# Kernel tuning notes

Hardware: AMD Instinct MI355X
Metric: run time of the kernel (lower is better)

The kernel has to match this reference:

```python
import jax, jax.numpy as jnp
import numpy as np

INITIAL_RADIUS = 1.0  # init_kwargs: initial_radius > 0 -> distance-softmax branch


def reference(xyz, sparse_xyz, sparse_flow, resol_factor, K):
    # xyz: [B,3,N], sparse_xyz: [B,3,M], sparse_flow: [B,3,M]
    q = jnp.transpose(xyz, (0, 2, 1))            # [B,N,3]
    p = jnp.transpose(sparse_xyz, (0, 2, 1))     # [B,M,3]
    flow = jnp.transpose(sparse_flow, (0, 2, 1))  # [B,M,3]

    sigma = INITIAL_RADIUS * resol_factor
    qs = q / sigma
    ps = p / sigma

    # pairwise Euclidean distances [B,N,M]
    sq = (jnp.sum(qs * qs, -1)[:, :, None]
          + jnp.sum(ps * ps, -1)[:, None, :]
          - 2.0 * jnp.einsum('bnc,bmc->bnm', qs, ps))
    dist = jnp.sqrt(jnp.maximum(sq, 1e-12))

    # K nearest: smallest distances
    neg_d, idx = jax.lax.top_k(-dist, K)          # [B,N,K]
    K_dist = -neg_d                               # [B,N,K]

    # gather flow of the K neighbors: [B,N,K,3]
    grouped_flow = jnp.take_along_axis(flow[:, None, :, :], idx[..., None], axis=2)

    # softmax over -distance along K, weighted sum
    K_w = jax.nn.softmax(-K_dist, axis=2)         # [B,N,K]
    dense_flow = jnp.sum(K_w[..., None] * grouped_flow, axis=2)  # [B,N,3]

    return jnp.transpose(dense_flow, (0, 2, 1))   # [B,3,N]


def setup_inputs() -> dict:
    key = jax.random.key(0)
    k1, k2, k3 = jax.random.split(key, 3)
    B, N, M = 4, 16384, 4096
    return {
        'xyz': jax.random.normal(k1, (B, 3, N), dtype=jnp.float32),
        'sparse_xyz': jax.random.normal(k2, (B, 3, M), dtype=jnp.float32),
        'sparse_flow': jax.random.normal(k3, (B, 3, M), dtype=jnp.float32),
        'resol_factor': 1,
        'K': 5,
    }
```

## Files before the change

kernel.cpp:

```cpp
#include <hip/hip_runtime.h>
#include <math.h>
#include <stdint.h>


#define KNN 5
#define GRID 8
#define NCELL (GRID * GRID * GRID)
#define SPAN_TH 64
#define SLICES 8
#define BLOCK (SLICES * 64)
#define EPSM 1e-3f

typedef unsigned int u32;

__device__ __forceinline__ float get_inv_sigma(const int* __restrict__ rf) {
    const int ri = rf[0];
    const float sigma = (ri >= 1 && ri <= 1000000) ? (float)ri : __int_as_float(ri);
    return 1.0f / sigma;
}

__device__ __forceinline__ float rfl_f(float v) {
    return __int_as_float(__builtin_amdgcn_readfirstlane(__float_as_int(v)));
}

__device__ __forceinline__ int cid1(float x, float lo, float ich) {
    const int c = (int)floorf((x - lo) * ich);
    return c < 0 ? 0 : (c > GRID - 1 ? GRID - 1 : c);
}

__device__ __forceinline__ int sp3(int v) {
    return (v & 1) | ((v & 2) << 2) | ((v & 4) << 4);
}

#define CE_FULL(k, ki, c, ci)                          \
    {                                                  \
        const bool sw = (c) < (k);                     \
        const float vmn = fminf(k, c);                 \
        const float vmx = fmaxf(k, c);                 \
        const u32 nki = sw ? (ci) : (ki);              \
        const u32 nci = sw ? (ki) : (ci);              \
        (k) = vmn; (c) = vmx; (ki) = nki; (ci) = nci;  \
    }
#define CE_LAST(k, ki, c, ci)                          \
    {                                                  \
        const bool sw = (c) < (k);                     \
        (ki) = sw ? (ci) : (ki);                       \
        (k) = fminf(k, c);                             \
    }

#define LAD(P, CI)                                     \
    {                                                  \
        float t_ = qx * (P).x;                         \
        t_ = fmaf(qy, (P).y, t_);                      \
        t_ = fmaf(qz, (P).z, t_);                      \
        float c_ = fmaf(-2.0f, t_, (P).w);             \
        u32 ci_ = (u32)(CI);                           \
        CE_FULL(e0, i0, c_, ci_)                       \
        CE_FULL(e1, i1, c_, ci_)                       \
        CE_FULL(e2, i2, c_, ci_)                       \
        CE_FULL(e3, i3, c_, ci_)                       \
        CE_LAST(e4, i4, c_, ci_)                       \
    }


__global__ __launch_bounds__(256)
void prep_kernel(const float* __restrict__ sxyz, const int* __restrict__ rf,
                 float4* __restrict__ pts, int M, int total) {
    const int t = blockIdx.x * 256 + threadIdx.x;
    if (t >= total) return;
    const float inv = get_inv_sigma(rf);
    const int b = t / M, m = t - b * M;
    const float* sb = sxyz + (size_t)b * 3 * M;
    const float x = sb[m] * inv;
    const float y = sb[M + m] * inv;
    const float z = sb[2 * M + m] * inv;
    pts[t] = make_float4(x, y, z, fmaf(x, x, fmaf(y, y, z * z)));
}

template <bool USE_PTS>
__global__ __launch_bounds__(BLOCK, 8)
void knn_kernel(const float* __restrict__ xyz,
                const float* __restrict__ sxyz,
                const float* __restrict__ sflow,
                const int* __restrict__ rf,
                const float4* __restrict__ pts,
                float* __restrict__ out,
                int N, int M) {
    __shared__ float sval_d[SLICES * KNN * 64];
    __shared__ u32   sval_i[SLICES * KNN * 64];

    const int tid  = threadIdx.x;
    const int lane = tid & 63;
    const int wid  = tid >> 6;
    const int swid = __builtin_amdgcn_readfirstlane(wid);
    const int gpb  = N / 64;
    const int b    = blockIdx.x / gpb;
    const int grp  = blockIdx.x - b * gpb;
    const int n    = grp * 64 + lane;

    const float inv = get_inv_sigma(rf);
    const float* qb = xyz + (size_t)b * 3 * N;
    const float qx = qb[n] * inv;
    const float qy = qb[N + n] * inv;
    const float qz = qb[2 * N + n] * inv;
    const float qq = fmaf(qx, qx, fmaf(qy, qy, qz * qz));

    const int CH = M / SLICES;
    const int j0 = swid * CH;

    float e0 = 1e30f, e1 = 1e30f, e2 = 1e30f, e3 = 1e30f, e4 = 1e30f;
    u32   i0 = 0, i1 = 0, i2 = 0, i3 = 0, i4 = 0;

    if constexpr (USE_PTS) {
        const float4* __restrict__ P = pts + (size_t)b * M + j0;
#pragma unroll 4
        for (int j = 0; j < CH; ++j) {
            const float4 p = P[j];
            LAD(p, j0 + j)
        }
    } else {
        const float* __restrict__ sb = sxyz + (size_t)b * 3 * M;
#pragma unroll 4
        for (int j = 0; j < CH; ++j) {
            const float px = sb[j0 + j] * inv;
            const float py = sb[M + j0 + j] * inv;
            const float pz = sb[2 * M + j0 + j] * inv;
            const float pw = fmaf(px, px, fmaf(py, py, pz * pz));
            const float4 p = make_float4(px, py, pz, pw);
            LAD(p, j0 + j)
        }
    }

    sval_d[(wid * KNN + 0) * 64 + lane] = e0;  sval_i[(wid * KNN + 0) * 64 + lane] = i0;
    sval_d[(wid * KNN + 1) * 64 + lane] = e1;  sval_i[(wid * KNN + 1) * 64 + lane] = i1;
    sval_d[(wid * KNN + 2) * 64 + lane] = e2;  sval_i[(wid * KNN + 2) * 64 + lane] = i2;
    sval_d[(wid * KNN + 3) * 64 + lane] = e3;  sval_i[(wid * KNN + 3) * 64 + lane] = i3;
    sval_d[(wid * KNN + 4) * 64 + lane] = e4;  sval_i[(wid * KNN + 4) * 64 + lane] = i4;
    __syncthreads();

    if (wid == 0) {
        float m0 = 1e30f, m1 = 1e30f, m2 = 1e30f, m3 = 1e30f, m4 = 1e30f;
        u32   g0 = 0, g1 = 0, g2 = 0, g3 = 0, g4 = 0;
#pragma unroll
        for (int w = 0; w < SLICES; ++w) {
#pragma unroll
            for (int k = 0; k < KNN; ++k) {
                float c = sval_d[(w * KNN + k) * 64 + lane];
                u32  ci = sval_i[(w * KNN + k) * 64 + lane];
                CE_FULL(m0, g0, c, ci)
                CE_FULL(m1, g1, c, ci)
                CE_FULL(m2, g2, c, ci)
                CE_FULL(m3, g3, c, ci)
                CE_LAST(m4, g4, c, ci)
            }
        }

        const float d0 = sqrtf(fmaxf(m0 + qq, 1e-12f));
        const float d1 = sqrtf(fmaxf(m1 + qq, 1e-12f));
        const float d2 = sqrtf(fmaxf(m2 + qq, 1e-12f));
        const float d3 = sqrtf(fmaxf(m3 + qq, 1e-12f));
        const float d4 = sqrtf(fmaxf(m4 + qq, 1e-12f));
        const float w0 = 1.0f;
        const float w1 = expf(d0 - d1);
        const float w2 = expf(d0 - d2);
        const float w3 = expf(d0 - d3);
        const float w4 = expf(d0 - d4);
        const float inv_wsum = 1.0f / (w0 + w1 + w2 + w3 + w4);

        const float* fb = sflow + (size_t)b * 3 * M;
        float ax = 0.f, ay = 0.f, az = 0.f;
        ax = fmaf(w0, fb[g0], ax); ay = fmaf(w0, fb[M + g0], ay); az = fmaf(w0, fb[2 * M + g0], az);
        ax = fmaf(w1, fb[g1], ax); ay = fmaf(w1, fb[M + g1], ay); az = fmaf(w1, fb[2 * M + g1], az);
        ax = fmaf(w2, fb[g2], ax); ay = fmaf(w2, fb[M + g2], ay); az = fmaf(w2, fb[2 * M + g2], az);
        ax = fmaf(w3, fb[g3], ax); ay = fmaf(w3, fb[M + g3], ay); az = fmaf(w3, fb[2 * M + g3], az);
        ax = fmaf(w4, fb[g4], ax); ay = fmaf(w4, fb[M + g4], ay); az = fmaf(w4, fb[2 * M + g4], az);

        float* ob = out + (size_t)b * 3 * N;
        ob[n]         = ax * inv_wsum;
        ob[N + n]     = ay * inv_wsum;
        ob[2 * N + n] = az * inv_wsum;
    }
}


__global__ __launch_bounds__(1024)
void prep_all_kernel(const float* __restrict__ xyz, const float* __restrict__ sxyz,
                     const int* __restrict__ rf, float* __restrict__ bbox,
                     int2* __restrict__ off2C, float4* __restrict__ ptsS,
                     float4* __restrict__ qS, int* __restrict__ idxS,
                     int N, int M) {
    __shared__ int hC[NCELL], hQ[NCELL];
    __shared__ int oC[NCELL], oQ[NCELL];
    __shared__ float sred[6][16];
    __shared__ float sbb[6];

    const int b = blockIdx.x, t = threadIdx.x;
    const int lane = t & 63, w = t >> 6;
    const float inv = get_inv_sigma(rf);
    const float* sb = sxyz + (size_t)b * 3 * M;
    const float* qb = xyz + (size_t)b * 3 * N;

    float lx = 1e30f, ly = 1e30f, lz = 1e30f, hx = -1e30f, hy = -1e30f, hz = -1e30f;
    for (int m = t; m < M; m += 1024) {
        const float x = sb[m] * inv, y = sb[M + m] * inv, z = sb[2 * M + m] * inv;
        lx = fminf(lx, x); hx = fmaxf(hx, x);
        ly = fminf(ly, y); hy = fmaxf(hy, y);
        lz = fminf(lz, z); hz = fmaxf(hz, z);
    }
#pragma unroll
    for (int mm = 1; mm < 64; mm <<= 1) {
        lx = fminf(lx, __shfl_xor(lx, mm, 64));
        ly = fminf(ly, __shfl_xor(ly, mm, 64));
        lz = fminf(lz, __shfl_xor(lz, mm, 64));
        hx = fmaxf(hx, __shfl_xor(hx, mm, 64));
        hy = fmaxf(hy, __shfl_xor(hy, mm, 64));
        hz = fmaxf(hz, __shfl_xor(hz, mm, 64));
    }
    if (lane == 0) {
        sred[0][w] = lx; sred[1][w] = ly; sred[2][w] = lz;
        sred[3][w] = hx; sred[4][w] = hy; sred[5][w] = hz;
    }
    for (int c = t; c < NCELL; c += 1024) { hC[c] = 0; hQ[c] = 0; }
    __syncthreads();
    if (t == 0) {
        float Lx = sred[0][0], Ly = sred[1][0], Lz = sred[2][0];
        float Hx = sred[3][0], Hy = sred[4][0], Hz = sred[5][0];
        for (int k = 1; k < 16; ++k) {
            Lx = fminf(Lx, sred[0][k]); Ly = fminf(Ly, sred[1][k]); Lz = fminf(Lz, sred[2][k]);
            Hx = fmaxf(Hx, sred[3][k]); Hy = fmaxf(Hy, sred[4][k]); Hz = fmaxf(Hz, sred[5][k]);
        }
        const float sc = (1.0f / GRID) * (1.0f + 4e-6f);
        sbb[0] = Lx; sbb[1] = Ly; sbb[2] = Lz;
        sbb[3] = (Hx - Lx) * sc + 1e-30f;
        sbb[4] = (Hy - Ly) * sc + 1e-30f;
        sbb[5] = (Hz - Lz) * sc + 1e-30f;
        for (int k = 0; k < 6; ++k) bbox[b * 8 + k] = sbb[k];
    }
    __syncthreads();
    const float lox = sbb[0], loy = sbb[1], loz = sbb[2];
    const float icx = 1.0f / sbb[3], icy = 1.0f / sbb[4], icz = 1.0f / sbb[5];

#define CELL_OF(X, Y, Z) \
    ((sp3(cid1((X), lox, icx)) << 2) | (sp3(cid1((Y), loy, icy)) << 1) | sp3(cid1((Z), loz, icz)))

    for (int m = t; m < M; m += 1024) {
        const float x = sb[m] * inv, y = sb[M + m] * inv, z = sb[2 * M + m] * inv;
        atomicAdd(&hC[CELL_OF(x, y, z)], 1);
    }
    for (int i = t; i < N; i += 1024) {
        const float x = qb[i] * inv, y = qb[N + i] * inv, z = qb[2 * N + i] * inv;
        atomicAdd(&hQ[CELL_OF(x, y, z)], 1);
    }
    __syncthreads();

    if (t < NCELL) { oC[t] = hC[t]; oQ[t] = hQ[t]; }
    __syncthreads();
    for (int d = 1; d < NCELL; d <<= 1) {
        int vc = 0, vq = 0;
        if (t < NCELL && t >= d) { vc = oC[t - d]; vq = oQ[t - d]; }
        __syncthreads();
        if (t < NCELL && t >= d) { oC[t] += vc; oQ[t] += vq; }
        __syncthreads();
    }
    if (t < NCELL) {
        const int e = oC[t], h = hC[t];
        off2C[(size_t)b * NCELL + t] = make_int2(e - h, e);
        oC[t] = e - h;
        oQ[t] = oQ[t] - hQ[t];
    }
    __syncthreads();

    for (int m = t; m < M; m += 1024) {
        const float x = sb[m] * inv, y = sb[M + m] * inv, z = sb[2 * M + m] * inv;
        const int slot = atomicAdd(&oC[CELL_OF(x, y, z)], 1);
        ptsS[(size_t)b * M + slot] = make_float4(x, y, z, fmaf(x, x, fmaf(y, y, z * z)));
        idxS[(size_t)b * M + slot] = m;
    }
    for (int i = t; i < N; i += 1024) {
        const float x = qb[i] * inv, y = qb[N + i] * inv, z = qb[2 * N + i] * inv;
        const int slot = atomicAdd(&oQ[CELL_OF(x, y, z)], 1);
        qS[(size_t)b * N + slot] = make_float4(x, y, z, __int_as_float(i));
    }
#undef CELL_OF
}


#define CELLP(CZ)                                                                   \
    {                                                                               \
        const float glz_ = fmaf((float)(CZ), chz, loz);                             \
        const float dz_ = fmaxf(fmaxf(glz_ - whz, wlz - (glz_ + chz)), 0.0f);       \
        const float dl_ = fmaf(dz_, dz_, dxy_);                                     \
        if (!(dl_ > TwR)) {                                                         \
            const int cell_ = mxy_ | sp3(CZ);                                       \
            const int2 oo_ = off2b[cell_];                                          \
            const int base_ = __builtin_amdgcn_readfirstlane(oo_.x);                \
            const int end_ = __builtin_amdgcn_readfirstlane(oo_.y);                 \
            int j_ = base_;                                                         \
            for (; j_ + 4 <= end_; j_ += 4) {                                       \
                const float4 p0_ = Pb[j_];                                          \
                const float4 p1_ = Pb[j_ + 1];                                      \
                const float4 p2_ = Pb[j_ + 2];                                      \
                const float4 p3_ = Pb[j_ + 3];                                      \
                LAD(p0_, j_) LAD(p1_, j_ + 1)                                       \
                LAD(p2_, j_ + 2) LAD(p3_, j_ + 3)                                   \
            }                                                                       \
            for (; j_ < end_; ++j_) {                                               \
                const float4 pp_ = Pb[j_];                                          \
                LAD(pp_, j_)                                                        \
            }                                                                       \
        }                                                                           \
    }

#define COLUMN(HAVEFULL)                                                            \
    {                                                                               \
        if (((colctr++) & 7) == wid) {                                              \
            TwR = fminf(TwOwn,                                                      \
                        __int_as_float(__hip_atomic_load(                           \
                            &twS, __ATOMIC_RELAXED, __HIP_MEMORY_SCOPE_WORKGROUP))); \
            const float gly_ = fmaf((float)cy, chy, loy);                           \
            const float dy_ = fmaxf(fmaxf(gly_ - why, wly - (gly_ + chy)), 0.0f);   \
            const float dxy_ = fmaf(dy_, dy_, dxx);                                 \
            if (!(dxy_ > TwR)) {                                                    \
                const int mxy_ = mx | (sp3(cy) << 1);                               \
                const float old4_ = e4;                                             \
                if (HAVEFULL) {                                                     \
                    for (int cz = z0; cz <= z1; ++cz) { CELLP(cz) }                 \
                } else {                                                            \
                    if (clz - r >= 0) { CELLP(clz - r) }                            \
                    if (czh + r <= GRID - 1) { CELLP(czh + r) }                     \
                }                                                                   \
                if (__any(e4 < old4_)) {                                            \
                    float m4_ = e4 + qq;                                            \
                    for (int mm_ = 1; mm_ < 64; mm_ <<= 1)                          \
                        m4_ = fmaxf(m4_, __shfl_xor(m4_, mm_, 64));                 \
                    m4_ = rfl_f(m4_);                                               \
                    TwOwn = fminf(TwOwn, m4_);                                      \
                    TwR = fminf(TwR, m4_);                                          \
                    if (lane == 0) atomicMin(&twS, __float_as_int(m4_));            \
                }                                                                   \
            }                                                                       \
        }                                                                           \
    }

__global__ __launch_bounds__(BLOCK, 8)
void knn_grid8_kernel(const float4* __restrict__ qS, const float4* __restrict__ ptsS,
                      const int* __restrict__ idxS, const int2* __restrict__ off2C,
                      const float* __restrict__ bbox, const float* __restrict__ sflow,
                      float* __restrict__ out, int N, int M) {
    __shared__ float sval_d[SLICES * KNN * 64];
    __shared__ u32   sval_i[SLICES * KNN * 64];
    __shared__ int   twS;

    const int tid  = threadIdx.x;
    const int lane = tid & 63;
    const int wid  = tid >> 6;
    const int swid = __builtin_amdgcn_readfirstlane(wid);
    const int gpb  = N >> 6;
    const int b    = blockIdx.x / gpb;
    const int grp  = blockIdx.x - b * gpb;

    if (tid == 0) twS = 0x7F800000;
    __syncthreads();

    const float4 q4 = qS[(size_t)b * N + grp * 64 + lane];
    const float qx = q4.x, qy = q4.y, qz = q4.z;
    const int n = __float_as_int(q4.w);
    const float qq = fmaf(qx, qx, fmaf(qy, qy, qz * qz));

    float wlx = qx, wly = qy, wlz = qz, whx = qx, why = qy, whz = qz;
#pragma unroll
    for (int m = 1; m < 64; m <<= 1) {
        wlx = fminf(wlx, __shfl_xor(wlx, m, 64));
        whx = fmaxf(whx, __shfl_xor(whx, m, 64));
        wly = fminf(wly, __shfl_xor(wly, m, 64));
        why = fmaxf(why, __shfl_xor(why, m, 64));
        wlz = fminf(wlz, __shfl_xor(wlz, m, 64));
        whz = fmaxf(whz, __shfl_xor(whz, m, 64));
    }
    wlx = rfl_f(wlx) - EPSM; whx = rfl_f(whx) + EPSM;
    wly = rfl_f(wly) - EPSM; why = rfl_f(why) + EPSM;
    wlz = rfl_f(wlz) - EPSM; whz = rfl_f(whz) + EPSM;

    const float* bb = bbox + b * 8;
    const float lox = bb[0], loy = bb[1], loz = bb[2];
    const float chx = bb[3], chy = bb[4], chz = bb[5];
    const float hmin = fminf(chx, fminf(chy, chz));

    const int clx = cid1(wlx, lox, 1.0f / chx), cxh = cid1(whx, lox, 1.0f / chx);
    const int cly = cid1(wly, loy, 1.0f / chy), cyh = cid1(why, loy, 1.0f / chy);
    const int clz = cid1(wlz, loz, 1.0f / chz), czh = cid1(whz, loz, 1.0f / chz);

    float e0 = 1e30f, e1 = 1e30f, e2 = 1e30f, e3 = 1e30f, e4 = 1e30f;
    u32   i0 = 0, i1 = 0, i2 = 0, i3 = 0, i4 = 0;

    const float4* __restrict__ Pb = ptsS + (size_t)b * M;
    const int2* __restrict__ off2b = off2C + (size_t)b * NCELL;

    const int span = (cxh - clx + 1) * (cyh - cly + 1) * (czh - clz + 1);
    if (span > SPAN_TH) {
        const int CH = M / SLICES;
        const int j0 = swid * CH;
        const float4* __restrict__ P = Pb + j0;
#pragma unroll 4
        for (int j = 0; j < CH; ++j) {
            const float4 p = P[j];
            LAD(p, j0 + j)
        }
    } else {
        float TwOwn = 1e30f, TwR = 1e30f;
        int colctr = 0;
        for (int r = 0; r <= GRID; ++r) {
            TwR = fminf(TwOwn, __int_as_float(__hip_atomic_load(
                                   &twS, __ATOMIC_RELAXED, __HIP_MEMORY_SCOPE_WORKGROUP)));
            if (r >= 2) {
                const float bd = (float)(r - 1) * hmin - EPSM;
                if (bd > 0.0f && bd * bd > TwR) break;
            }
            const int x0 = clx - r < 0 ? 0 : clx - r;
            const int x1 = cxh + r > GRID - 1 ? GRID - 1 : cxh + r;
            const int y0 = cly - r < 0 ? 0 : cly - r;
            const int y1 = cyh + r > GRID - 1 ? GRID - 1 : cyh + r;
            const int z0 = clz - r < 0 ? 0 : clz - r;
            const int z1 = czh + r > GRID - 1 ? GRID - 1 : czh + r;
            for (int cx = x0; cx <= x1; ++cx) {
                const int rx = cx < clx ? clx - cx : (cx > cxh ? cx - cxh : 0);
                const float glx = fmaf((float)cx, chx, lox);
                const float dx = fmaxf(fmaxf(glx - whx, wlx - (glx + chx)), 0.0f);
                const float dxx = dx * dx;
                const int mx = sp3(cx) << 2;
                for (int cy = y0; cy <= y1; ++cy) {
                    const int ry = cy < cly ? cly - cy : (cy > cyh ? cy - cyh : 0);
                    if ((rx > ry ? rx : ry) == r) {
                        COLUMN(true)
                    } else {
                        COLUMN(false)
                    }
                }
            }
        }
    }

    sval_d[(wid * KNN + 0) * 64 + lane] = e0;  sval_i[(wid * KNN + 0) * 64 + lane] = i0;
    sval_d[(wid * KNN + 1) * 64 + lane] = e1;  sval_i[(wid * KNN + 1) * 64 + lane] = i1;
    sval_d[(wid * KNN + 2) * 64 + lane] = e2;  sval_i[(wid * KNN + 2) * 64 + lane] = i2;
    sval_d[(wid * KNN + 3) * 64 + lane] = e3;  sval_i[(wid * KNN + 3) * 64 + lane] = i3;
    sval_d[(wid * KNN + 4) * 64 + lane] = e4;  sval_i[(wid * KNN + 4) * 64 + lane] = i4;
    __syncthreads();

    if (wid == 0) {
        float m0 = 1e30f, m1 = 1e30f, m2 = 1e30f, m3 = 1e30f, m4 = 1e30f;
        u32 g0 = 0, g1 = 0, g2 = 0, g3 = 0, g4 = 0;
#pragma unroll
        for (int w = 0; w < SLICES; ++w) {
#pragma unroll
            for (int k = 0; k < KNN; ++k) {
                float c = sval_d[(w * KNN + k) * 64 + lane];
                u32 ci = sval_i[(w * KNN + k) * 64 + lane];
                CE_FULL(m0, g0, c, ci)
                CE_FULL(m1, g1, c, ci)
                CE_FULL(m2, g2, c, ci)
                CE_FULL(m3, g3, c, ci)
                CE_LAST(m4, g4, c, ci)
            }
        }

        const float d0 = sqrtf(fmaxf(m0 + qq, 1e-12f));
        const float d1 = sqrtf(fmaxf(m1 + qq, 1e-12f));
        const float d2 = sqrtf(fmaxf(m2 + qq, 1e-12f));
        const float d3 = sqrtf(fmaxf(m3 + qq, 1e-12f));
        const float d4 = sqrtf(fmaxf(m4 + qq, 1e-12f));
        const float w0 = 1.0f;
        const float w1 = expf(d0 - d1);
        const float w2 = expf(d0 - d2);
        const float w3 = expf(d0 - d3);
        const float w4 = expf(d0 - d4);
        const float inv_wsum = 1.0f / (w0 + w1 + w2 + w3 + w4);

        const int* __restrict__ idxb = idxS + (size_t)b * M;
        const int o0 = idxb[g0], o1 = idxb[g1], o2 = idxb[g2], o3 = idxb[g3], o4 = idxb[g4];
        const float* fb = sflow + (size_t)b * 3 * M;
        float ax = 0.f, ay = 0.f, az = 0.f;
        ax = fmaf(w0, fb[o0], ax); ay = fmaf(w0, fb[M + o0], ay); az = fmaf(w0, fb[2 * M + o0], az);
        ax = fmaf(w1, fb[o1], ax); ay = fmaf(w1, fb[M + o1], ay); az = fmaf(w1, fb[2 * M + o1], az);
        ax = fmaf(w2, fb[o2], ax); ay = fmaf(w2, fb[M + o2], ay); az = fmaf(w2, fb[2 * M + o2], az);
        ax = fmaf(w3, fb[o3], ax); ay = fmaf(w3, fb[M + o3], ay); az = fmaf(w3, fb[2 * M + o3], az);
        ax = fmaf(w4, fb[o4], ax); ay = fmaf(w4, fb[M + o4], ay); az = fmaf(w4, fb[2 * M + o4], az);

        float* ob = out + (size_t)b * 3 * N;
        ob[n]         = ax * inv_wsum;
        ob[N + n]     = ay * inv_wsum;
        ob[2 * N + n] = az * inv_wsum;
    }
}

extern "C" void kernel_launch(void* const* d_in, const int* in_sizes, int n_in,
                              void* d_out, int out_size, void* d_ws, size_t ws_size,
                              hipStream_t stream) {
    const float* xyz   = (const float*)d_in[0];
    const float* sxyz  = (const float*)d_in[1];
    const float* sflow = (const float*)d_in[2];
    const int*   rf    = (const int*)d_in[3];

    const int B = 4;
    const int N = in_sizes[0] / (3 * B);
    const int M = in_sizes[1] / (3 * B);
    float* out = (float*)d_out;

    size_t o = 0;
    float4* ptsS  = (float4*)((char*)d_ws + o); o += (size_t)B * M * sizeof(float4);
    float4* qS    = (float4*)((char*)d_ws + o); o += (size_t)B * N * sizeof(float4);
    int*   idxS   = (int*)((char*)d_ws + o);    o += (size_t)B * M * 4;
    float* bbox   = (float*)((char*)d_ws + o);  o += 256;
    int2*  off2C  = (int2*)((char*)d_ws + o);   o += (size_t)B * NCELL * 8;
    const size_t need = o;

    if (ws_size >= need && (N % 64) == 0 && (M % (8 * SLICES)) == 0) {
        prep_all_kernel<<<dim3(B), dim3(1024), 0, stream>>>(
            xyz, sxyz, rf, bbox, off2C, ptsS, qS, idxS, N, M);
        knn_grid8_kernel<<<dim3(B * (N / 64)), dim3(BLOCK), 0, stream>>>(
            qS, ptsS, idxS, off2C, bbox, sflow, out, N, M);
    } else {
        const dim3 grid(B * (N / 64));
        const dim3 block(BLOCK);
        const size_t needOld = (size_t)B * M * sizeof(float4);
        if (ws_size >= needOld) {
            float4* pts = (float4*)d_ws;
            prep_kernel<<<dim3((B * M + 255) / 256), dim3(256), 0, stream>>>(
                sxyz, rf, pts, M, B * M);
            knn_kernel<true><<<grid, block, 0, stream>>>(xyz, sxyz, sflow, rf, pts, out, N, M);
        } else {
            knn_kernel<false><<<grid, block, 0, stream>>>(xyz, sxyz, sflow, rf, nullptr, out, N, M);
        }
    }
}
```

Before: 312.9 us.

## Split grid prep into parallel multi-block kernels and restructure KNN cell search

The single-block-per-batch prep kernel is replaced by four grid-wide kernels: bbox reduction with encoded-float atomics, histogram with global atomics, per-slice scan, and scatter. This is meant to remove the serial prep bottleneck where only B blocks of 1024 threads did all binning. The KNN kernel also drops the shared atomic threshold in favour of first visiting the window's own cells, then reducing a bound across slices. Later rings are pruned with per-lane point-to-cell distance tests. The change adds several launches and global atomics, and the pruning now relies on a slightly loosened epsilon tolerance.

```diff
diff --git a/kernel.cpp b/kernel.cpp
--- a/kernel.cpp
+++ b/kernel.cpp
@@ -30,6 +30,28 @@
 
 __device__ __forceinline__ int sp3(int v) {
     return (v & 1) | ((v & 2) << 2) | ((v & 4) << 4);
+}
+
+__device__ __forceinline__ u32 fenc(float f) {
+    const u32 b = __float_as_uint(f);
+    return (b & 0x80000000u) ? ~b : (b | 0x80000000u);
+}
+__device__ __forceinline__ float fdec(u32 u) {
+    return __uint_as_float((u & 0x80000000u) ? (u & 0x7FFFFFFFu) : ~u);
+}
+
+__device__ __forceinline__ void bb_load(const u32* __restrict__ minU,
+                                        const u32* __restrict__ maxU, int b,
+                                        float& lox, float& loy, float& loz,
+                                        float& chx, float& chy, float& chz) {
+    const float sc = (1.0f / GRID) * (1.0f + 4e-6f);
+    const float Lx = fdec(minU[b * 3 + 0]);
+    const float Ly = fdec(minU[b * 3 + 1]);
+    const float Lz = fdec(minU[b * 3 + 2]);
+    lox = Lx; loy = Ly; loz = Lz;
+    chx = (fdec(maxU[b * 3 + 0]) - Lx) * sc + 1e-30f;
+    chy = (fdec(maxU[b * 3 + 1]) - Ly) * sc + 1e-30f;
+    chz = (fdec(maxU[b * 3 + 2]) - Lz) * sc + 1e-30f;
 }
 
 #define CE_FULL(k, ki, c, ci)                          \
@@ -183,30 +205,16 @@
 }
 
 
-__global__ __launch_bounds__(1024)
-void prep_all_kernel(const float* __restrict__ xyz, const float* __restrict__ sxyz,
-                     const int* __restrict__ rf, float* __restrict__ bbox,
-                     int2* __restrict__ off2C, float4* __restrict__ ptsS,
-                     float4* __restrict__ qS, int* __restrict__ idxS,
-                     int N, int M) {
-    __shared__ int hC[NCELL], hQ[NCELL];
-    __shared__ int oC[NCELL], oQ[NCELL];
-    __shared__ float sred[6][16];
-    __shared__ float sbb[6];
-
-    const int b = blockIdx.x, t = threadIdx.x;
-    const int lane = t & 63, w = t >> 6;
+__global__ __launch_bounds__(256)
+void bbox_atomic_kernel(const float* __restrict__ sxyz, const int* __restrict__ rf,
+                        u32* __restrict__ minU, u32* __restrict__ maxU, int M) {
+    const int per = M / 256;
+    const int b = blockIdx.x / per;
+    const int m = (blockIdx.x - b * per) * 256 + threadIdx.x;
     const float inv = get_inv_sigma(rf);
     const float* sb = sxyz + (size_t)b * 3 * M;
-    const float* qb = xyz + (size_t)b * 3 * N;
-
-    float lx = 1e30f, ly = 1e30f, lz = 1e30f, hx = -1e30f, hy = -1e30f, hz = -1e30f;
-    for (int m = t; m < M; m += 1024) {
-        const float x = sb[m] * inv, y = sb[M + m] * inv, z = sb[2 * M + m] * inv;
-        lx = fminf(lx, x); hx = fmaxf(hx, x);
-        ly = fminf(ly, y); hy = fmaxf(hy, y);
-        lz = fminf(lz, z); hz = fmaxf(hz, z);
-    }
+    const float x = sb[m] * inv, y = sb[M + m] * inv, z = sb[2 * M + m] * inv;
+    float lx = x, ly = y, lz = z, hx = x, hy = y, hz = z;
 #pragma unroll
     for (int mm = 1; mm < 64; mm <<= 1) {
         lx = fminf(lx, __shfl_xor(lx, mm, 64));
@@ -216,140 +224,140 @@
         hy = fmaxf(hy, __shfl_xor(hy, mm, 64));
         hz = fmaxf(hz, __shfl_xor(hz, mm, 64));
     }
-    if (lane == 0) {
-        sred[0][w] = lx; sred[1][w] = ly; sred[2][w] = lz;
-        sred[3][w] = hx; sred[4][w] = hy; sred[5][w] = hz;
-    }
-    for (int c = t; c < NCELL; c += 1024) { hC[c] = 0; hQ[c] = 0; }
-    __syncthreads();
-    if (t == 0) {
-        float Lx = sred[0][0], Ly = sred[1][0], Lz = sred[2][0];
-        float Hx = sred[3][0], Hy = sred[4][0], Hz = sred[5][0];
-        for (int k = 1; k < 16; ++k) {
-            Lx = fminf(Lx, sred[0][k]); Ly = fminf(Ly, sred[1][k]); Lz = fminf(Lz, sred[2][k]);
-            Hx = fmaxf(Hx, sred[3][k]); Hy = fmaxf(Hy, sred[4][k]); Hz = fmaxf(Hz, sred[5][k]);
-        }
-        const float sc = (1.0f / GRID) * (1.0f + 4e-6f);
-        sbb[0] = Lx; sbb[1] = Ly; sbb[2] = Lz;
-        sbb[3] = (Hx - Lx) * sc + 1e-30f;
-        sbb[4] = (Hy - Ly) * sc + 1e-30f;
-        sbb[5] = (Hz - Lz) * sc + 1e-30f;
-        for (int k = 0; k < 6; ++k) bbox[b * 8 + k] = sbb[k];
-    }
-    __syncthreads();
-    const float lox = sbb[0], loy = sbb[1], loz = sbb[2];
-    const float icx = 1.0f / sbb[3], icy = 1.0f / sbb[4], icz = 1.0f / sbb[5];
-
-#define CELL_OF(X, Y, Z) \
-    ((sp3(cid1((X), lox, icx)) << 2) | (sp3(cid1((Y), loy, icy)) << 1) | sp3(cid1((Z), loz, icz)))
-
-    for (int m = t; m < M; m += 1024) {
-        const float x = sb[m] * inv, y = sb[M + m] * inv, z = sb[2 * M + m] * inv;
-        atomicAdd(&hC[CELL_OF(x, y, z)], 1);
-    }
-    for (int i = t; i < N; i += 1024) {
-        const float x = qb[i] * inv, y = qb[N + i] * inv, z = qb[2 * N + i] * inv;
-        atomicAdd(&hQ[CELL_OF(x, y, z)], 1);
-    }
-    __syncthreads();
-
-    if (t < NCELL) { oC[t] = hC[t]; oQ[t] = hQ[t]; }
+    if ((threadIdx.x & 63) == 0) {
+        atomicMin(&minU[b * 3 + 0], fenc(lx));
+        atomicMin(&minU[b * 3 + 1], fenc(ly));
+        atomicMin(&minU[b * 3 + 2], fenc(lz));
+        atomicMax(&maxU[b * 3 + 0], fenc(hx));
+        atomicMax(&maxU[b * 3 + 1], fenc(hy));
+        atomicMax(&maxU[b * 3 + 2], fenc(hz));
+    }
+}
+
+__global__ __launch_bounds__(256)
+void hist_kernel2(const float* __restrict__ xyz, const float* __restrict__ sxyz,
+                  const int* __restrict__ rf, const u32* __restrict__ minU,
+                  const u32* __restrict__ maxU, int* __restrict__ histAll,
+                  int N, int M, int B) {
+    const int t = blockIdx.x * 256 + threadIdx.x;
+    const int TC = B * M;
+    const float inv = get_inv_sigma(rf);
+    float x, y, z; int b, slice;
+    if (t < TC) {
+        b = t / M; const int i = t - b * M;
+        const float* sb = sxyz + (size_t)b * 3 * M;
+        x = sb[i] * inv; y = sb[M + i] * inv; z = sb[2 * M + i] * inv;
+        slice = b;
+    } else if (t < TC + B * N) {
+        const int t2 = t - TC;
+        b = t2 / N; const int i = t2 - b * N;
+        const float* qb = xyz + (size_t)b * 3 * N;
+        x = qb[i] * inv; y = qb[N + i] * inv; z = qb[2 * N + i] * inv;
+        slice = B + b;
+    } else return;
+    float lox, loy, loz, chx, chy, chz;
+    bb_load(minU, maxU, b, lox, loy, loz, chx, chy, chz);
+    const int cell = (sp3(cid1(x, lox, 1.0f / chx)) << 2) |
+                     (sp3(cid1(y, loy, 1.0f / chy)) << 1) |
+                      sp3(cid1(z, loz, 1.0f / chz));
+    atomicAdd(&histAll[(size_t)slice * NCELL + cell], 1);
+}
+
+__global__ __launch_bounds__(NCELL)
+void scan_kernel2(const int* __restrict__ histAll, int2* __restrict__ off2C,
+                  int* __restrict__ curAll, int B) {
+    __shared__ int sc[NCELL];
+    const int s = blockIdx.x;
+    const int t = threadIdx.x;
+    const int h = histAll[(size_t)s * NCELL + t];
+    sc[t] = h;
     __syncthreads();
     for (int d = 1; d < NCELL; d <<= 1) {
-        int vc = 0, vq = 0;
-        if (t < NCELL && t >= d) { vc = oC[t - d]; vq = oQ[t - d]; }
+        const int v = (t >= d) ? sc[t - d] : 0;
         __syncthreads();
-        if (t < NCELL && t >= d) { oC[t] += vc; oQ[t] += vq; }
+        sc[t] += v;
         __syncthreads();
     }
-    if (t < NCELL) {
-        const int e = oC[t], h = hC[t];
-        off2C[(size_t)b * NCELL + t] = make_int2(e - h, e);
-        oC[t] = e - h;
-        oQ[t] = oQ[t] - hQ[t];
-    }
-    __syncthreads();
-
-    for (int m = t; m < M; m += 1024) {
-        const float x = sb[m] * inv, y = sb[M + m] * inv, z = sb[2 * M + m] * inv;
-        const int slot = atomicAdd(&oC[CELL_OF(x, y, z)], 1);
+    const int excl = sc[t] - h;
+    curAll[(size_t)s * NCELL + t] = excl;
+    if (s < B) off2C[(size_t)s * NCELL + t] = make_int2(excl, excl + h);
+}
+
+__global__ __launch_bounds__(256)
+void scatter_kernel2(const float* __restrict__ xyz, const float* __restrict__ sxyz,
+                     const int* __restrict__ rf, const u32* __restrict__ minU,
+                     const u32* __restrict__ maxU, int* __restrict__ curAll,
+                     float4* __restrict__ ptsS, float4* __restrict__ qS,
+                     int* __restrict__ idxS, int N, int M, int B) {
+    const int t = blockIdx.x * 256 + threadIdx.x;
+    const int TC = B * M;
+    const float inv = get_inv_sigma(rf);
+    float x, y, z; int b, i, slice;
+    bool isQ;
+    if (t < TC) {
+        b = t / M; i = t - b * M;
+        const float* sb = sxyz + (size_t)b * 3 * M;
+        x = sb[i] * inv; y = sb[M + i] * inv; z = sb[2 * M + i] * inv;
+        slice = b; isQ = false;
+    } else if (t < TC + B * N) {
+        const int t2 = t - TC;
+        b = t2 / N; i = t2 - b * N;
+        const float* qb = xyz + (size_t)b * 3 * N;
+        x = qb[i] * inv; y = qb[N + i] * inv; z = qb[2 * N + i] * inv;
+        slice = B + b; isQ = true;
+    } else return;
+    float lox, loy, loz, chx, chy, chz;
+    bb_load(minU, maxU, b, lox, loy, loz, chx, chy, chz);
+    const int cell = (sp3(cid1(x, lox, 1.0f / chx)) << 2) |
+                     (sp3(cid1(y, loy, 1.0f / chy)) << 1) |
+                      sp3(cid1(z, loz, 1.0f / chz));
+    const int slot = atomicAdd(&curAll[(size_t)slice * NCELL + cell], 1);
+    if (isQ) {
+        qS[(size_t)b * N + slot] = make_float4(x, y, z, __int_as_float(i));
+    } else {
         ptsS[(size_t)b * M + slot] = make_float4(x, y, z, fmaf(x, x, fmaf(y, y, z * z)));
-        idxS[(size_t)b * M + slot] = m;
-    }
-    for (int i = t; i < N; i += 1024) {
-        const float x = qb[i] * inv, y = qb[N + i] * inv, z = qb[2 * N + i] * inv;
-        const int slot = atomicAdd(&oQ[CELL_OF(x, y, z)], 1);
-        qS[(size_t)b * N + slot] = make_float4(x, y, z, __int_as_float(i));
-    }
-#undef CELL_OF
-}
-
-
-#define CELLP(CZ)                                                                   \
-    {                                                                               \
-        const float glz_ = fmaf((float)(CZ), chz, loz);                             \
-        const float dz_ = fmaxf(fmaxf(glz_ - whz, wlz - (glz_ + chz)), 0.0f);       \
-        const float dl_ = fmaf(dz_, dz_, dxy_);                                     \
-        if (!(dl_ > TwR)) {                                                         \
-            const int cell_ = mxy_ | sp3(CZ);                                       \
-            const int2 oo_ = off2b[cell_];                                          \
-            const int base_ = __builtin_amdgcn_readfirstlane(oo_.x);                \
-            const int end_ = __builtin_amdgcn_readfirstlane(oo_.y);                 \
-            int j_ = base_;                                                         \
-            for (; j_ + 4 <= end_; j_ += 4) {                                       \
-                const float4 p0_ = Pb[j_];                                          \
-                const float4 p1_ = Pb[j_ + 1];                                      \
-                const float4 p2_ = Pb[j_ + 2];                                      \
-                const float4 p3_ = Pb[j_ + 3];                                      \
-                LAD(p0_, j_) LAD(p1_, j_ + 1)                                       \
-                LAD(p2_, j_ + 2) LAD(p3_, j_ + 3)                                   \
-            }                                                                       \
-            for (; j_ < end_; ++j_) {                                               \
-                const float4 pp_ = Pb[j_];                                          \
-                LAD(pp_, j_)                                                        \
-            }                                                                       \
-        }                                                                           \
-    }
-
-#define COLUMN(HAVEFULL)                                                            \
-    {                                                                               \
-        if (((colctr++) & 7) == wid) {                                              \
-            TwR = fminf(TwOwn,                                                      \
-                        __int_as_float(__hip_atomic_load(                           \
-                            &twS, __ATOMIC_RELAXED, __HIP_MEMORY_SCOPE_WORKGROUP))); \
-            const float gly_ = fmaf((float)cy, chy, loy);                           \
-            const float dy_ = fmaxf(fmaxf(gly_ - why, wly - (gly_ + chy)), 0.0f);   \
-            const float dxy_ = fmaf(dy_, dy_, dxx);                                 \
-            if (!(dxy_ > TwR)) {                                                    \
-                const int mxy_ = mx | (sp3(cy) << 1);                               \
-                const float old4_ = e4;                                             \
-                if (HAVEFULL) {                                                     \
-                    for (int cz = z0; cz <= z1; ++cz) { CELLP(cz) }                 \
-                } else {                                                            \
-                    if (clz - r >= 0) { CELLP(clz - r) }                            \
-                    if (czh + r <= GRID - 1) { CELLP(czh + r) }                     \
-                }                                                                   \
-                if (__any(e4 < old4_)) {                                            \
-                    float m4_ = e4 + qq;                                            \
-                    for (int mm_ = 1; mm_ < 64; mm_ <<= 1)                          \
-                        m4_ = fmaxf(m4_, __shfl_xor(m4_, mm_, 64));                 \
-                    m4_ = rfl_f(m4_);                                               \
-                    TwOwn = fminf(TwOwn, m4_);                                      \
-                    TwR = fminf(TwR, m4_);                                          \
-                    if (lane == 0) atomicMin(&twS, __float_as_int(m4_));            \
-                }                                                                   \
-            }                                                                       \
-        }                                                                           \
+        idxS[(size_t)b * M + slot] = i;
+    }
+}
+
+
+#define CELLP(CZ)                                                               \
+    {                                                                           \
+        const float glz_ = fmaf((float)(CZ), chz, loz);                         \
+        const float cqz_ = fminf(fmaxf(qz, glz_), glz_ + chz);                  \
+        const float dzl_ = qz - cqz_;                                           \
+        const float d3_ = fmaf(dzl_, dzl_, dxy2);                               \
+        const float cmp_ = fmaf(e4 + qq, 1.00001f, EPSM);                       \
+        if (!__all(d3_ > cmp_)) {                                               \
+            const int cell_ = mxy | sp3(CZ);                                    \
+            const int2 oo_ = off2b[cell_];                                      \
+            const int base_ = __builtin_amdgcn_readfirstlane(oo_.x);            \
+            const int end_ = __builtin_amdgcn_readfirstlane(oo_.y);             \
+            int j_ = base_;                                                     \
+            for (; j_ + 4 <= end_; j_ += 4) {                                   \
+                const float4 p0_ = Pb[j_];                                      \
+                const float4 p1_ = Pb[j_ + 1];                                  \
+                const float4 p2_ = Pb[j_ + 2];                                  \
+                const float4 p3_ = Pb[j_ + 3];                                  \
+                LAD(p0_, j_) LAD(p1_, j_ + 1)                                   \
+                LAD(p2_, j_ + 2) LAD(p3_, j_ + 3)                               \
+            }                                                                   \
+            for (; j_ < end_; ++j_) {                                           \
+                const float4 pp_ = Pb[j_];                                      \
+                LAD(pp_, j_)                                                    \
+            }                                                                   \
+        }                                                                       \
     }
 
 __global__ __launch_bounds__(BLOCK, 8)
 void knn_grid8_kernel(const float4* __restrict__ qS, const float4* __restrict__ ptsS,
                       const int* __restrict__ idxS, const int2* __restrict__ off2C,
-                      const float* __restrict__ bbox, const float* __restrict__ sflow,
+                      const u32* __restrict__ minU, const u32* __restrict__ maxU,
+                      const float* __restrict__ sflow,
                       float* __restrict__ out, int N, int M) {
     __shared__ float sval_d[SLICES * KNN * 64];
     __shared__ u32   sval_i[SLICES * KNN * 64];
-    __shared__ int   twS;
+    __shared__ float se4[SLICES * 64];
 
     const int tid  = threadIdx.x;
     const int lane = tid & 63;
@@ -359,9 +367,6 @@
     const int b    = blockIdx.x / gpb;
     const int grp  = blockIdx.x - b * gpb;
 
-    if (tid == 0) twS = 0x7F800000;
-    __syncthreads();
-
     const float4 q4 = qS[(size_t)b * N + grp * 64 + lane];
     const float qx = q4.x, qy = q4.y, qz = q4.z;
     const int n = __float_as_int(q4.w);
@@ -381,9 +386,8 @@
     wly = rfl_f(wly) - EPSM; why = rfl_f(why) + EPSM;
     wlz = rfl_f(wlz) - EPSM; whz = rfl_f(whz) + EPSM;
 
-    const float* bb = bbox + b * 8;
-    const float lox = bb[0], loy = bb[1], loz = bb[2];
-    const float chx = bb[3], chy = bb[4], chz = bb[5];
+    float lox, loy, loz, chx, chy, chz;
+    bb_load(minU, maxU, b, lox, loy, loz, chx, chy, chz);
     const float hmin = fminf(chx, fminf(chy, chz));
 
     const int clx = cid1(wlx, lox, 1.0f / chx), cxh = cid1(whx, lox, 1.0f / chx);
@@ -407,14 +411,42 @@
             LAD(p, j0 + j)
         }
     } else {
-        float TwOwn = 1e30f, TwR = 1e30f;
-        int colctr = 0;
-        for (int r = 0; r <= GRID; ++r) {
-            TwR = fminf(TwOwn, __int_as_float(__hip_atomic_load(
-                                   &twS, __ATOMIC_RELAXED, __HIP_MEMORY_SCOPE_WORKGROUP)));
+        int ctr = 0;
+        for (int cx = clx; cx <= cxh; ++cx) {
+            const float glx = fmaf((float)cx, chx, lox);
+            const float cqx = fminf(fmaxf(qx, glx), glx + chx);
+            const float dxl = qx - cqx;
+            const float dxx = dxl * dxl;
+            const int mx = sp3(cx) << 2;
+            for (int cy = cly; cy <= cyh; ++cy) {
+                const float gly = fmaf((float)cy, chy, loy);
+                const float cqy = fminf(fmaxf(qy, gly), gly + chy);
+                const float dyl = qy - cqy;
+                const float dxy2 = fmaf(dyl, dyl, dxx);
+                const int mxy = mx | (sp3(cy) << 1);
+                for (int cz = clz; cz <= czh; ++cz) {
+                    if (((ctr++) & 7) == wid) { CELLP(cz) }
+                }
+            }
+        }
+        se4[wid * 64 + lane] = e4;
+        __syncthreads();
+        float bnd = se4[lane];
+#pragma unroll
+        for (int w = 1; w < SLICES; ++w) bnd = fminf(bnd, se4[w * 64 + lane]);
+        bnd += qq;
+#pragma unroll
+        for (int mm = 1; mm < 64; mm <<= 1) bnd = fmaxf(bnd, __shfl_xor(bnd, mm, 64));
+        float TwR = rfl_f(bnd);
+
+        for (int r = 1; r <= GRID; ++r) {
+            float own = e4 + qq;
+#pragma unroll
+            for (int mm = 1; mm < 64; mm <<= 1) own = fmaxf(own, __shfl_xor(own, mm, 64));
+            TwR = fminf(TwR, rfl_f(own));
             if (r >= 2) {
                 const float bd = (float)(r - 1) * hmin - EPSM;
-                if (bd > 0.0f && bd * bd > TwR) break;
+                if (bd > 0.0f && bd * bd > fmaf(TwR, 1.00001f, EPSM)) break;
             }
             const int x0 = clx - r < 0 ? 0 : clx - r;
             const int x1 = cxh + r > GRID - 1 ? GRID - 1 : cxh + r;
@@ -425,15 +457,27 @@
             for (int cx = x0; cx <= x1; ++cx) {
                 const int rx = cx < clx ? clx - cx : (cx > cxh ? cx - cxh : 0);
                 const float glx = fmaf((float)cx, chx, lox);
-                const float dx = fmaxf(fmaxf(glx - whx, wlx - (glx + chx)), 0.0f);
-                const float dxx = dx * dx;
+                const float cqx = fminf(fmaxf(qx, glx), glx + chx);
+                const float dxl = qx - cqx;
+                const float dxx = dxl * dxl;
                 const int mx = sp3(cx) << 2;
                 for (int cy = y0; cy <= y1; ++cy) {
                     const int ry = cy < cly ? cly - cy : (cy > cyh ? cy - cyh : 0);
-                    if ((rx > ry ? rx : ry) == r) {
-                        COLUMN(true)
-                    } else {
-                        COLUMN(false)
+                    if (((ctr++) & 7) == wid) {
+                        const float gly = fmaf((float)cy, chy, loy);
+                        const float cqy = fminf(fmaxf(qy, gly), gly + chy);
+                        const float dyl = qy - cqy;
+                        const float dxy2 = fmaf(dyl, dyl, dxx);
+                        const float cmpc = fmaf(e4 + qq, 1.00001f, EPSM);
+                        if (!__all(dxy2 > cmpc)) {
+                            const int mxy = mx | (sp3(cy) << 1);
+                            if ((rx > ry ? rx : ry) == r) {
+                                for (int cz = z0; cz <= z1; ++cz) { CELLP(cz) }
+                            } else {
+                                if (clz - r >= 0) { CELLP(clz - r) }
+                                if (czh + r <= GRID - 1) { CELLP(czh + r) }
+                            }
+                        }
                     }
                 }
             }
@@ -510,15 +554,27 @@
     float4* ptsS  = (float4*)((char*)d_ws + o); o += (size_t)B * M * sizeof(float4);
     float4* qS    = (float4*)((char*)d_ws + o); o += (size_t)B * N * sizeof(float4);
     int*   idxS   = (int*)((char*)d_ws + o);    o += (size_t)B * M * 4;
-    float* bbox   = (float*)((char*)d_ws + o);  o += 256;
+    u32*   minU   = (u32*)((char*)d_ws + o);    o += (size_t)B * 3 * 4;
+    u32*   maxU   = (u32*)((char*)d_ws + o);    o += (size_t)B * 3 * 4;
+    int*   histAll= (int*)((char*)d_ws + o);    o += (size_t)2 * B * NCELL * 4;
+    int*   curAll = (int*)((char*)d_ws + o);    o += (size_t)2 * B * NCELL * 4;
     int2*  off2C  = (int2*)((char*)d_ws + o);   o += (size_t)B * NCELL * 8;
     const size_t need = o;
 
-    if (ws_size >= need && (N % 64) == 0 && (M % (8 * SLICES)) == 0) {
-        prep_all_kernel<<<dim3(B), dim3(1024), 0, stream>>>(
-            xyz, sxyz, rf, bbox, off2C, ptsS, qS, idxS, N, M);
+    if (ws_size >= need && (N % 64) == 0 && (M % 256) == 0) {
+        const int total = B * (M + N);
+        hipMemsetAsync(minU, 0xFF, (size_t)B * 3 * 4, stream);
+        hipMemsetAsync(maxU, 0x00, (size_t)B * 3 * 4 + (size_t)2 * B * NCELL * 4, stream);
+        bbox_atomic_kernel<<<dim3(B * (M / 256)), dim3(256), 0, stream>>>(
+            sxyz, rf, minU, maxU, M);
+        hist_kernel2<<<dim3((total + 255) / 256), dim3(256), 0, stream>>>(
+            xyz, sxyz, rf, minU, maxU, histAll, N, M, B);
+        scan_kernel2<<<dim3(2 * B), dim3(NCELL), 0, stream>>>(
+            histAll, off2C, curAll, B);
+        scatter_kernel2<<<dim3((total + 255) / 256), dim3(256), 0, stream>>>(
+            xyz, sxyz, rf, minU, maxU, curAll, ptsS, qS, idxS, N, M, B);
         knn_grid8_kernel<<<dim3(B * (N / 64)), dim3(BLOCK), 0, stream>>>(
-            qS, ptsS, idxS, off2C, bbox, sflow, out, N, M);
+            qS, ptsS, idxS, off2C, minU, maxU, sflow, out, N, M);
     } else {
         const dim3 grid(B * (N / 64));
         const dim3 block(BLOCK);
```

After: 269.5 us. 1.16x faster.
